# Performance work log

Hardware: AMD Instinct MI355X
Metric: run time of the kernel (lower is better)

Reference implementation:

```python
import jax, jax.numpy as jnp
import numpy as np

D = 1024      # d_model
E = 8         # num_experts
K = 2         # top_k
H = 4096      # expert_dim (bottleneck)
P = 256       # proj_dim
BATCH, SEQ = 2, 2048
CLAMP_MAX = float(np.log(1.0 / 0.01))
INIT_T = 0.5


def setup_inputs() -> dict:
    key = jax.random.key(0)
    ks = jax.random.split(key, 6)
    x = jax.random.normal(ks[0], (BATCH, SEQ, D), jnp.float32)
    # cosine projector (nn.Linear default init ~ U(-1/sqrt(D), 1/sqrt(D)))
    lim = 1.0 / np.sqrt(D)
    Wp = jax.random.uniform(ks[1], (P, D), jnp.float32, -lim, lim)
    bp = jnp.zeros((P,), jnp.float32)
    sim = 0.01 * jax.random.normal(ks[2], (P, E), jnp.float32)
    temp = jnp.full((1,), np.log(1.0 / INIT_T), jnp.float32)
    # RepAdapter 1x1 convs == linear layers; xavier_uniform, zero bias
    bA = float(np.sqrt(6.0 / (D + H)))
    A = jax.random.uniform(ks[3], (E, H, D), jnp.float32, -bA, bA)
    a_bias = jnp.zeros((E, H), jnp.float32)
    Bw = jax.random.uniform(ks[4], (E, D, H), jnp.float32, -bA, bA)
    b_bias = jnp.zeros((E, D), jnp.float32)
    return dict(x=x, Wp=Wp, bp=bp, sim=sim, temp=temp, A=A, a_bias=a_bias, Bw=Bw, b_bias=b_bias)


def reference(x, Wp, bp, sim, temp, A, a_bias, Bw, b_bias):
    B, S, d = x.shape
    e = sim.shape[1]
    xf = x.reshape(-1, d)                                  # [T, D]
    # cosine gate
    proj = xf @ Wp.T + bp                                  # [T, P]
    projn = proj / jnp.maximum(jnp.linalg.norm(proj, axis=1, keepdims=True), 1e-12)
    simn = sim / jnp.maximum(jnp.linalg.norm(sim, axis=0, keepdims=True), 1e-12)
    scale = jnp.exp(jnp.minimum(temp, CLAMP_MAX))          # [1]
    gate_probs = jax.nn.softmax((projn @ simn) * scale, axis=-1)   # [T, E]
    topv, topi = jax.lax.top_k(gate_probs, K)              # [T, K]
    topv = topv / (topv.sum(axis=-1, keepdims=True) + 1e-8)
    # per-token per-expert combine weight
    w = jnp.sum(topv[:, :, None] * jax.nn.one_hot(topi, e, dtype=x.dtype), axis=1)  # [T, E]

    # experts: y_e(x) = x + B_e(A_e x + a_e) + b_e (no nonlinearity); combine weighted
    def body(acc, params):
        Ae, ab, Be, bb, we = params
        h = xf @ Ae.T + ab                                 # [T, H]
        f = h @ Be.T + bb                                  # [T, D]
        return acc + we[:, None] * (xf + f), None

    out, _ = jax.lax.scan(body, jnp.zeros_like(xf), (A, a_bias, Bw, b_bias, w.T))
    out = out.reshape(B, S, d)

    frac = gate_probs.mean(axis=0)                         # expert_fractions
    aux_loss = jnp.sum((frac - 1.0 / e) ** 2)
    usage = jnp.bincount(topi.reshape(-1), length=e).astype(jnp.float32)
    return out, aux_loss, frac, usage
```

## Files before the change

### kernel.cpp

```cpp
#include <hip/hip_runtime.h>
#include <stdint.h>


typedef __attribute__((ext_vector_type(4))) float floatx4;
typedef __attribute__((ext_vector_type(8))) short shortx8;
typedef unsigned short ushort_t;

#define T_TOKENS 4096
#define D_DIM    1024
#define E_EXP    8
#define H_DIM    4096
#define P_DIM    256
#define ROWS_PAD 10240
#define MBLK     40
#define MBLK1    80

__device__ __forceinline__ ushort_t f2bf(float f) {
  union { float f; unsigned int u; } c; c.f = f;
  unsigned int u = c.u;
  unsigned int r = u + 0x7FFFu + ((u >> 16) & 1u);
  return (ushort_t)(r >> 16);
}

__device__ __forceinline__ void stage16(const ushort_t* g, ushort_t* l) {
  __builtin_amdgcn_global_load_lds((const __attribute__((address_space(1))) void*)g,
                                   (__attribute__((address_space(3))) void*)l, 16, 0, 0);
}

__global__ __launch_bounds__(256) void k_cvt(const float* __restrict__ src,
                                             ushort_t* __restrict__ dst, int n4) {
  int g = blockIdx.x * 256 + threadIdx.x;
  if (g >= n4) return;
  floatx4 v = ((const floatx4*)src)[g];
  ushort4 o; o.x = f2bf(v.x); o.y = f2bf(v.y); o.z = f2bf(v.z); o.w = f2bf(v.w);
  ((ushort4*)dst)[g] = o;
}

__global__ __launch_bounds__(256) void k_small_init(int* counts, int* cursor,
                                                    float* frac_sum, int* row2tok) {
  int g = blockIdx.x * 256 + threadIdx.x;
  if (g < 8) { counts[g] = 0; cursor[g] = 0; frac_sum[g] = 0.f; }
  if (g < ROWS_PAD) row2tok[g] = -1;
}

__global__ __launch_bounds__(256) void k_proj(const float* __restrict__ x,
                                              const float* __restrict__ Wp,
                                              const float* __restrict__ bp,
                                              float* __restrict__ proj) {
  __shared__ float Wc[256 * 36];
  __shared__ float Xc[16 * 36];
  int tid = threadIdx.x;
  int t0 = blockIdx.x * 16;
  int cg = tid & 31, tg = tid >> 5;
  floatx4 acc[2][8];
#pragma unroll
  for (int a = 0; a < 2; a++)
#pragma unroll
    for (int b = 0; b < 8; b++) acc[a][b] = (floatx4){0.f, 0.f, 0.f, 0.f};
  for (int kc = 0; kc < 32; ++kc) {
    int k0 = kc * 32;
    __syncthreads();
#pragma unroll
    for (int it = 0; it < 8; ++it) {
      int f = it * 256 + tid;
      int j = f >> 3, kk = (f & 7) << 2;
      floatx4 v = *(const floatx4*)(Wp + j * 1024 + k0 + kk);
      *(floatx4*)(Wc + j * 36 + kk) = v;
    }
    if (tid < 128) {
      int t = tid >> 3, kk = (tid & 7) << 2;
      floatx4 v = *(const floatx4*)(x + (size_t)(t0 + t) * 1024 + k0 + kk);
      *(floatx4*)(Xc + t * 36 + kk) = v;
    }
    __syncthreads();
#pragma unroll
    for (int k4 = 0; k4 < 8; ++k4) {
      floatx4 xv[2], wv[8];
#pragma unroll
      for (int tt = 0; tt < 2; tt++) xv[tt] = *(floatx4*)(Xc + (tg * 2 + tt) * 36 + k4 * 4);
#pragma unroll
      for (int jj = 0; jj < 8; jj++) wv[jj] = *(floatx4*)(Wc + (cg + jj * 32) * 36 + k4 * 4);
#pragma unroll
      for (int tt = 0; tt < 2; tt++)
#pragma unroll
        for (int jj = 0; jj < 8; jj++) acc[tt][jj] += xv[tt] * wv[jj];
    }
  }
#pragma unroll
  for (int tt = 0; tt < 2; tt++)
#pragma unroll
    for (int jj = 0; jj < 8; jj++) {
      floatx4 a = acc[tt][jj];
      float s = (a.x + a.y) + (a.z + a.w);
      int t = t0 + tg * 2 + tt, j = cg + jj * 32;
      proj[t * 256 + j] = s + bp[j];
    }
}

__global__ __launch_bounds__(128) void k_gate(const float* __restrict__ proj,
                                              const float* __restrict__ sim,
                                              const float* __restrict__ temp,
                                              int* __restrict__ topi, float* __restrict__ wslot,
                                              float* __restrict__ swsum,
                                              float* __restrict__ frac_sum, int* __restrict__ counts) {
  __shared__ float simT[8][256];
  __shared__ float snorm[8];
  __shared__ float fracs[8];
  __shared__ int cnts[8];
  int tid = threadIdx.x;
  for (int i = tid; i < 2048; i += 128) { int p = i >> 3, e = i & 7; simT[e][p] = sim[i]; }
  if (tid < 8) { fracs[tid] = 0.f; cnts[tid] = 0; }
  __syncthreads();
  if (tid < 8) {
    float s = 0.f;
    for (int p = 0; p < 256; p++) { float v = simT[tid][p]; s += v * v; }
    snorm[tid] = fmaxf(sqrtf(s), 1e-12f);
  }
  __syncthreads();
  int t = blockIdx.x * 128 + tid;
  floatx4 n4 = (floatx4){0.f, 0.f, 0.f, 0.f};
  floatx4 d4[8];
#pragma unroll
  for (int e = 0; e < 8; e++) d4[e] = (floatx4){0.f, 0.f, 0.f, 0.f};
  const floatx4* pr = (const floatx4*)(proj + t * 256);
  for (int k4 = 0; k4 < 64; ++k4) {
    floatx4 p = pr[k4];
    n4 += p * p;
#pragma unroll
    for (int e = 0; e < 8; e++) d4[e] += p * *(const floatx4*)(&simT[e][k4 * 4]);
  }
  float nrm = fmaxf(sqrtf((n4.x + n4.y) + (n4.z + n4.w)), 1e-12f);
  float scale = expf(fminf(temp[0], 4.6051701859880914f));
  float pe[8];
  float mx = -1e30f;
#pragma unroll
  for (int e = 0; e < 8; e++) {
    float d = (d4[e].x + d4[e].y) + (d4[e].z + d4[e].w);
    pe[e] = d / (nrm * snorm[e]) * scale;
    mx = fmaxf(mx, pe[e]);
  }
  float sum = 0.f;
#pragma unroll
  for (int e = 0; e < 8; e++) { pe[e] = expf(pe[e] - mx); sum += pe[e]; }
#pragma unroll
  for (int e = 0; e < 8; e++) pe[e] /= sum;
  int i0 = 0;
#pragma unroll
  for (int e = 1; e < 8; e++) if (pe[e] > pe[i0]) i0 = e;
  int i1 = (i0 == 0) ? 1 : 0;
#pragma unroll
  for (int e = 0; e < 8; e++) if (e != i1 && e != i0 && pe[e] > pe[i1]) i1 = e;
  float v0 = pe[i0], v1 = pe[i1];
  float s2 = v0 + v1 + 1e-8f;
  float w0 = v0 / s2, w1 = v1 / s2;
  topi[t * 2] = i0; topi[t * 2 + 1] = i1;
  wslot[t * 2] = w0; wslot[t * 2 + 1] = w1;
  swsum[t] = w0 + w1;
#pragma unroll
  for (int e = 0; e < 8; e++) atomicAdd(&fracs[e], pe[e]);
  atomicAdd(&cnts[i0], 1); atomicAdd(&cnts[i1], 1);
  __syncthreads();
  if (tid < 8) { atomicAdd(&frac_sum[tid], fracs[tid]); atomicAdd(&counts[tid], cnts[tid]); }
}

__global__ void k_scan(const int* __restrict__ counts, const float* __restrict__ frac_sum,
                       int* __restrict__ offsets, int* __restrict__ blk2e,
                       float* __restrict__ out_tail) {
  __shared__ int offs[9];
  if (threadIdx.x == 0) {
    int off = 0;
    for (int e = 0; e < 8; e++) { offs[e] = off; off += ((counts[e] + 255) >> 8) << 8; }
    offs[8] = off;
    for (int e = 0; e < 9; e++) offsets[e] = offs[e];
    float aux = 0.f;
    for (int e = 0; e < 8; e++) { float fr = frac_sum[e] / 4096.f; aux += (fr - 0.125f) * (fr - 0.125f); }
    out_tail[0] = aux;
  }
  __syncthreads();
  int tid = threadIdx.x;
  if (tid < MBLK) {
    int r = tid * 256, e = -1;
    for (int q = 0; q < 8; q++) if (r >= offs[q] && r < offs[q + 1]) e = q;
    blk2e[tid] = e;
  }
  if (tid < 8) {
    out_tail[1 + tid] = frac_sum[tid] / 4096.f;
    out_tail[9 + tid] = (float)counts[tid];
  }
}

__global__ __launch_bounds__(256) void k_assign(const int* __restrict__ topi,
                                                const float* __restrict__ wslot,
                                                const int* __restrict__ offsets,
                                                int* __restrict__ cursor,
                                                int* __restrict__ row2tok, float* __restrict__ roww) {
  int g = blockIdx.x * 256 + threadIdx.x;
  if (g >= 8192) return;
  int t = g >> 1;
  int e = topi[g];
  int pos = atomicAdd(&cursor[e], 1);
  int r = offsets[e] + pos;
  row2tok[r] = t;
  roww[r] = wslot[g];
}

__global__ __launch_bounds__(64) void k_gather(const float* __restrict__ x,
                                               const int* __restrict__ row2tok,
                                               ushort_t* __restrict__ xg) {
  int r = blockIdx.x;
  int t = row2tok[r];
  ushort4* dst = (ushort4*)(xg + (size_t)r * 1024);
  if (t < 0) {
    ushort4 z; z.x = z.y = z.z = z.w = 0;
    for (int i = threadIdx.x; i < 256; i += 64) dst[i] = z;
  } else {
    const floatx4* src = (const floatx4*)(x + (size_t)t * 1024);
    for (int i = threadIdx.x; i < 256; i += 64) {
      floatx4 v = src[i];
      ushort4 o; o.x = f2bf(v.x); o.y = f2bf(v.y); o.z = f2bf(v.z); o.w = f2bf(v.w);
      dst[i] = o;
    }
  }
}

__global__ __launch_bounds__(256) void k_init_out(const float* __restrict__ x,
                                                  const float* __restrict__ swsum,
                                                  float* __restrict__ out) {
  int g = blockIdx.x * 256 + threadIdx.x;
  float s = swsum[g >> 8];
  floatx4 v = ((const floatx4*)x)[g];
  ((floatx4*)out)[g] = v * s;
}

__global__ __launch_bounds__(256, 2) void k_gemm1(const ushort_t* __restrict__ Aop0,
                                                  const ushort_t* __restrict__ Wall,
                                                  const float* __restrict__ bias,
                                                  const int* __restrict__ blk2e,
                                                  ushort_t* __restrict__ hout) {
  const int K = 1024, N = 4096;
  int gx = gridDim.x;
  int nwg = gx * gridDim.y;
  int flat = blockIdx.y * gx + blockIdx.x;
  int qq = nwg >> 3, rr = nwg & 7;
  int xcd = flat & 7, idx = flat >> 3;
  int swz = (xcd < rr ? xcd * (qq + 1) : rr * (qq + 1) + (xcd - rr) * qq) + idx;
  int rb = swz / gx, nb = swz - rb * gx;
  int e = blk2e[rb >> 1];
  if (e < 0) return;
  const ushort_t* Aop = Aop0 + (size_t)rb * 128 * K;
  const ushort_t* Bop = Wall + (size_t)e * N * K + (size_t)nb * 128 * K;

  __shared__ ushort_t As[2][8192], Bs[2][8192];

  int tid = threadIdx.x, lane = tid & 63, wv = tid >> 6;
  int l15 = lane & 15, q = lane >> 4;
  int wm = (wv & 1) << 6, wn = (wv >> 1) << 6;
  floatx4 acc[4][4];
#pragma unroll
  for (int i = 0; i < 4; i++)
#pragma unroll
    for (int j = 0; j < 4; j++) acc[i][j] = (floatx4){0.f, 0.f, 0.f, 0.f};

  int srow = tid >> 3, schunk = tid & 7;

  auto stage = [&](int kt, int buf) {
#pragma unroll
    for (int r = 0; r < 4; ++r) {
      int row = (r << 5) + srow;
      size_t goff = (size_t)row * K + (size_t)(kt << 6) + (size_t)((schunk ^ (row & 7)) << 3);
      int loff = ((r << 8) + (wv << 6)) << 3;
      stage16(Aop + goff, &As[buf][loff]);
      stage16(Bop + goff, &Bs[buf][loff]);
    }
  };

  stage(0, 0);
  __syncthreads();
  int cur = 0;
  for (int kt = 0; kt < 16; ++kt) {
    if (kt + 1 < 16) stage(kt + 1, cur ^ 1);
    const ushort_t* Ab = As[cur];
    const ushort_t* Bb = Bs[cur];
#pragma unroll
    for (int kc = 0; kc < 2; ++kc) {
      int cw = (kc << 2) + q;
      shortx8 af[4], bfv[4];
#pragma unroll
      for (int i = 0; i < 4; ++i) {
        int row = wm + i * 16 + l15;
        af[i] = *(const shortx8*)(Ab + (row << 6) + ((cw ^ (row & 7)) << 3));
      }
#pragma unroll
      for (int j = 0; j < 4; ++j) {
        int row = wn + j * 16 + l15;
        bfv[j] = *(const shortx8*)(Bb + (row << 6) + ((cw ^ (row & 7)) << 3));
      }
#pragma unroll
      for (int i = 0; i < 4; ++i)
#pragma unroll
        for (int j = 0; j < 4; ++j)
          acc[i][j] = __builtin_amdgcn_mfma_f32_16x16x32_bf16(af[i], bfv[j], acc[i][j], 0, 0, 0);
    }
    __syncthreads();
    cur ^= 1;
  }

  const float* be = bias + (size_t)e * N + (size_t)nb * 128;
  ushort_t* hp = hout + (size_t)(rb * 128) * N + (size_t)nb * 128;
#pragma unroll
  for (int j = 0; j < 4; ++j) {
    int n = wn + j * 16 + l15;
    float bv = be[n];
#pragma unroll
    for (int i = 0; i < 4; ++i)
#pragma unroll
      for (int r = 0; r < 4; ++r) {
        int m = wm + i * 16 + (q << 2) + r;
        hp[(size_t)m * N + n] = f2bf(acc[i][j][r] + bv);
      }
  }
}

__global__ __launch_bounds__(512, 2) void k_gemm2(const ushort_t* __restrict__ Aop0,
                                                  const ushort_t* __restrict__ Wall,
                                                  const float* __restrict__ bias,
                                                  const int* __restrict__ blk2e,
                                                  int K, int N,
                                                  float* __restrict__ outp,
                                                  const int* __restrict__ row2tok,
                                                  const float* __restrict__ roww) {
  int gx = gridDim.x;
  int nwg = gx * gridDim.y;
  int flat = blockIdx.y * gx + blockIdx.x;
  int qq = nwg >> 3, rr = nwg & 7;
  int xcd = flat & 7, idx = flat >> 3;
  int swz = (xcd < rr ? xcd * (qq + 1) : rr * (qq + 1) + (xcd - rr) * qq) + idx;
  int rb = swz / gx, nb = swz - rb * gx;

  int e = blk2e[rb];
  if (e < 0) return;
  int Kslice = K / gridDim.z;
  int kbase = blockIdx.z * Kslice;
  const ushort_t* Aop = Aop0 + (size_t)rb * 256 * K + kbase;
  const ushort_t* Bop = Wall + (size_t)e * N * K + (size_t)nb * 256 * K + kbase;

  __shared__ ushort_t As[2][16384], Bs[2][16384];

  int tid = threadIdx.x, lane = tid & 63, wv = tid >> 6;
  int l15 = lane & 15, q = lane >> 4;
  int wm = (wv >> 2) << 7;
  int wn = (wv & 3) << 6;

  floatx4 acc[8][4];
#pragma unroll
  for (int i = 0; i < 8; i++)
#pragma unroll
    for (int j = 0; j < 4; j++) acc[i][j] = (floatx4){0.f, 0.f, 0.f, 0.f};

  int srow = tid >> 3;
  int schunk = tid & 7;
  int ksteps = Kslice >> 6;
  int cur = 0;

  auto stage = [&](int kt, int buf) {
#pragma unroll
    for (int r = 0; r < 4; ++r) {
      int row = (r << 6) + srow;
      size_t goff = (size_t)row * K + (size_t)(kt << 6) + (size_t)((schunk ^ (row & 7)) << 3);
      int loff = ((r << 9) + (wv << 6)) << 3;
      stage16(Aop + goff, &As[buf][loff]);
      stage16(Bop + goff, &Bs[buf][loff]);
    }
  };

  stage(0, 0);
  __syncthreads();
  for (int ks = 0; ks < ksteps; ++ks) {
    if (ks + 1 < ksteps) stage(ks + 1, cur ^ 1);
    const ushort_t* Ab = As[cur];
    const ushort_t* Bb = Bs[cur];
#pragma unroll
    for (int kc = 0; kc < 2; ++kc) {
      int cw = (kc << 2) + q;
      shortx8 af[8], bfv[4];
#pragma unroll
      for (int i = 0; i < 8; ++i) {
        int row = wm + i * 16 + l15;
        af[i] = *(const shortx8*)(Ab + (row << 6) + ((cw ^ (row & 7)) << 3));
      }
#pragma unroll
      for (int j = 0; j < 4; ++j) {
        int row = wn + j * 16 + l15;
        bfv[j] = *(const shortx8*)(Bb + (row << 6) + ((cw ^ (row & 7)) << 3));
      }
#pragma unroll
      for (int i = 0; i < 8; ++i)
#pragma unroll
        for (int j = 0; j < 4; ++j)
          acc[i][j] = __builtin_amdgcn_mfma_f32_16x16x32_bf16(af[i], bfv[j], acc[i][j], 0, 0, 0);
    }
    __syncthreads();
    cur ^= 1;
  }

  const float* be = bias + (size_t)e * N + (size_t)nb * 256;
  bool addb = (blockIdx.z == 0);
  float bvv[4];
#pragma unroll
  for (int j = 0; j < 4; ++j) bvv[j] = addb ? be[wn + j * 16 + l15] : 0.f;
#pragma unroll
  for (int i = 0; i < 8; ++i)
#pragma unroll
    for (int r = 0; r < 4; ++r) {
      int m = wm + i * 16 + (q << 2) + r;
      int grow = rb * 256 + m;
      int tok = row2tok[grow];
      if (tok < 0) continue;
      float w = roww[grow];
      float* op = outp + (size_t)tok * 1024 + nb * 256;
#pragma unroll
      for (int j = 0; j < 4; ++j) {
        int n = wn + j * 16 + l15;
        atomicAdd(op + n, (acc[i][j][r] + bvv[j]) * w);
      }
    }
}

extern "C" void kernel_launch(void* const* d_in, const int* in_sizes, int n_in,
                              void* d_out, int out_size, void* d_ws, size_t ws_size,
                              hipStream_t stream) {
  (void)in_sizes; (void)n_in; (void)out_size; (void)ws_size;
  const float* x      = (const float*)d_in[0];
  const float* Wp     = (const float*)d_in[1];
  const float* bp     = (const float*)d_in[2];
  const float* sim    = (const float*)d_in[3];
  const float* temp   = (const float*)d_in[4];
  const float* A      = (const float*)d_in[5];
  const float* a_bias = (const float*)d_in[6];
  const float* Bw     = (const float*)d_in[7];
  const float* b_bias = (const float*)d_in[8];
  float* out = (float*)d_out;

  char* ws = (char*)d_ws;
  ushort_t* Abf    = (ushort_t*)(ws);
  ushort_t* Bbf    = (ushort_t*)(ws + 67108864);
  ushort_t* xg     = (ushort_t*)(ws + 134217728);
  ushort_t* h      = (ushort_t*)(ws + 155189248);
  float*    proj   = (float*)   (ws + 239075328);
  int*      topi   = (int*)     (ws + 243269632);
  float*    wslot  = (float*)   (ws + 243302400);
  float*    swsum  = (float*)   (ws + 243335168);
  int*      row2tok= (int*)     (ws + 243351552);
  float*    roww   = (float*)   (ws + 243392512);
  int*      counts = (int*)     (ws + 243433472);
  int*      cursor = (int*)     (ws + 243433504);
  int*      offsets= (int*)     (ws + 243433536);
  int*      blk2e  = (int*)     (ws + 243433600);
  float*    fracs  = (float*)   (ws + 243433760);

  k_cvt<<<32768, 256, 0, stream>>>(A,  Abf, 8388608);
  k_cvt<<<32768, 256, 0, stream>>>(Bw, Bbf, 8388608);
  k_small_init<<<40, 256, 0, stream>>>(counts, cursor, fracs, row2tok);
  k_proj<<<256, 256, 0, stream>>>(x, Wp, bp, proj);
  k_gate<<<32, 128, 0, stream>>>(proj, sim, temp, topi, wslot, swsum, fracs, counts);
  k_scan<<<1, 128, 0, stream>>>(counts, fracs, offsets, blk2e, out + 4194304);
  k_assign<<<32, 256, 0, stream>>>(topi, wslot, offsets, cursor, row2tok, roww);
  k_gather<<<ROWS_PAD, 64, 0, stream>>>(x, row2tok, xg);
  k_init_out<<<4096, 256, 0, stream>>>(x, swsum, out);
  k_gemm1<<<dim3(32, MBLK1, 1), 256, 0, stream>>>(xg, Abf, a_bias, blk2e, h);
  k_gemm2<<<dim3(4, MBLK, 2), 512, 0, stream>>>(h, Bbf, b_bias, blk2e, 4096, 1024,
                                                out, row2tok, roww);
}
```

Measured before the change: 773.9 us.

## Shrink gemm2 tiles to 128x128 single-buffered, merge cvt launches, widen gather blocks

The second expert GEMM moves from 256x256 tiles with 512 threads and double-buffered LDS to 128x128 tiles with 256 threads, a single LDS buffer and more resident blocks per CU. The aim is more blocks and better occupancy to hide latency, but it gives up both the copy/compute overlap and the reuse per loaded tile. The two weight conversion kernels become one launch. The gather kernel now handles four rows per 256-thread block.

Result: faster. 736.5 us (-4.8%).

```diff
diff --git a/kernel.cpp b/kernel.cpp
--- a/kernel.cpp
+++ b/kernel.cpp
@@ -27,13 +27,17 @@
                                    (__attribute__((address_space(3))) void*)l, 16, 0, 0);
 }
 
-__global__ __launch_bounds__(256) void k_cvt(const float* __restrict__ src,
-                                             ushort_t* __restrict__ dst, int n4) {
+__global__ __launch_bounds__(256) void k_cvt2(const float* __restrict__ srcA,
+                                              const float* __restrict__ srcB,
+                                              ushort_t* __restrict__ dstA,
+                                              ushort_t* __restrict__ dstB) {
   int g = blockIdx.x * 256 + threadIdx.x;
-  if (g >= n4) return;
-  floatx4 v = ((const floatx4*)src)[g];
+  const float* s; ushort_t* d; int i;
+  if (g < 8388608) { s = srcA; d = dstA; i = g; }
+  else             { s = srcB; d = dstB; i = g - 8388608; }
+  floatx4 v = ((const floatx4*)s)[i];
   ushort4 o; o.x = f2bf(v.x); o.y = f2bf(v.y); o.z = f2bf(v.z); o.w = f2bf(v.w);
-  ((ushort4*)dst)[g] = o;
+  ((ushort4*)d)[i] = o;
 }
 
 __global__ __launch_bounds__(256) void k_small_init(int* counts, int* cursor,
@@ -204,18 +208,19 @@
   roww[r] = wslot[g];
 }
 
-__global__ __launch_bounds__(64) void k_gather(const float* __restrict__ x,
-                                               const int* __restrict__ row2tok,
-                                               ushort_t* __restrict__ xg) {
-  int r = blockIdx.x;
+__global__ __launch_bounds__(256) void k_gather(const float* __restrict__ x,
+                                                const int* __restrict__ row2tok,
+                                                ushort_t* __restrict__ xg) {
+  int r = blockIdx.x * 4 + (threadIdx.x >> 6);
+  int l = threadIdx.x & 63;
   int t = row2tok[r];
   ushort4* dst = (ushort4*)(xg + (size_t)r * 1024);
   if (t < 0) {
     ushort4 z; z.x = z.y = z.z = z.w = 0;
-    for (int i = threadIdx.x; i < 256; i += 64) dst[i] = z;
+    for (int i = l; i < 256; i += 64) dst[i] = z;
   } else {
     const floatx4* src = (const floatx4*)(x + (size_t)t * 1024);
-    for (int i = threadIdx.x; i < 256; i += 64) {
+    for (int i = l; i < 256; i += 64) {
       floatx4 v = src[i];
       ushort4 o; o.x = f2bf(v.x); o.y = f2bf(v.y); o.z = f2bf(v.z); o.w = f2bf(v.w);
       dst[i] = o;
@@ -321,7 +326,7 @@
   }
 }
 
-__global__ __launch_bounds__(512, 2) void k_gemm2(const ushort_t* __restrict__ Aop0,
+__global__ __launch_bounds__(256, 4) void k_gemm2(const ushort_t* __restrict__ Aop0,
                                                   const ushort_t* __restrict__ Wall,
                                                   const float* __restrict__ bias,
                                                   const int* __restrict__ blk2e,
@@ -337,93 +342,78 @@
   int swz = (xcd < rr ? xcd * (qq + 1) : rr * (qq + 1) + (xcd - rr) * qq) + idx;
   int rb = swz / gx, nb = swz - rb * gx;
 
-  int e = blk2e[rb];
+  int e = blk2e[rb >> 1];
   if (e < 0) return;
   int Kslice = K / gridDim.z;
   int kbase = blockIdx.z * Kslice;
-  const ushort_t* Aop = Aop0 + (size_t)rb * 256 * K + kbase;
-  const ushort_t* Bop = Wall + (size_t)e * N * K + (size_t)nb * 256 * K + kbase;
-
-  __shared__ ushort_t As[2][16384], Bs[2][16384];
+  const ushort_t* Aop = Aop0 + (size_t)rb * 128 * K + kbase;
+  const ushort_t* Bop = Wall + (size_t)e * N * K + (size_t)nb * 128 * K + kbase;
+
+  __shared__ ushort_t As[8192], Bs[8192];
 
   int tid = threadIdx.x, lane = tid & 63, wv = tid >> 6;
   int l15 = lane & 15, q = lane >> 4;
-  int wm = (wv >> 2) << 7;
-  int wn = (wv & 3) << 6;
-
-  floatx4 acc[8][4];
-#pragma unroll
-  for (int i = 0; i < 8; i++)
+  int wm = (wv & 1) << 6, wn = (wv >> 1) << 6;
+  floatx4 acc[4][4];
+#pragma unroll
+  for (int i = 0; i < 4; i++)
 #pragma unroll
     for (int j = 0; j < 4; j++) acc[i][j] = (floatx4){0.f, 0.f, 0.f, 0.f};
 
-  int srow = tid >> 3;
-  int schunk = tid & 7;
+  int srow = tid >> 3, schunk = tid & 7;
   int ksteps = Kslice >> 6;
-  int cur = 0;
-
-  auto stage = [&](int kt, int buf) {
+
+  for (int kt = 0; kt < ksteps; ++kt) {
 #pragma unroll
     for (int r = 0; r < 4; ++r) {
-      int row = (r << 6) + srow;
+      int row = (r << 5) + srow;
       size_t goff = (size_t)row * K + (size_t)(kt << 6) + (size_t)((schunk ^ (row & 7)) << 3);
-      int loff = ((r << 9) + (wv << 6)) << 3;
-      stage16(Aop + goff, &As[buf][loff]);
-      stage16(Bop + goff, &Bs[buf][loff]);
-    }
-  };
-
-  stage(0, 0);
-  __syncthreads();
-  for (int ks = 0; ks < ksteps; ++ks) {
-    if (ks + 1 < ksteps) stage(ks + 1, cur ^ 1);
-    const ushort_t* Ab = As[cur];
-    const ushort_t* Bb = Bs[cur];
+      int loff = ((r << 8) + (wv << 6)) << 3;
+      stage16(Aop + goff, &As[loff]);
+      stage16(Bop + goff, &Bs[loff]);
+    }
+    __syncthreads();
 #pragma unroll
     for (int kc = 0; kc < 2; ++kc) {
       int cw = (kc << 2) + q;
-      shortx8 af[8], bfv[4];
-#pragma unroll
-      for (int i = 0; i < 8; ++i) {
+      shortx8 af[4], bfv[4];
+#pragma unroll
+      for (int i = 0; i < 4; ++i) {
         int row = wm + i * 16 + l15;
-        af[i] = *(const shortx8*)(Ab + (row << 6) + ((cw ^ (row & 7)) << 3));
+        af[i] = *(const shortx8*)(As + (row << 6) + ((cw ^ (row & 7)) << 3));
       }
 #pragma unroll
       for (int j = 0; j < 4; ++j) {
         int row = wn + j * 16 + l15;
-        bfv[j] = *(const shortx8*)(Bb + (row << 6) + ((cw ^ (row & 7)) << 3));
-      }
-#pragma unroll
-      for (int i = 0; i < 8; ++i)
+        bfv[j] = *(const shortx8*)(Bs + (row << 6) + ((cw ^ (row & 7)) << 3));
+      }
+#pragma unroll
+      for (int i = 0; i < 4; ++i)
 #pragma unroll
         for (int j = 0; j < 4; ++j)
           acc[i][j] = __builtin_amdgcn_mfma_f32_16x16x32_bf16(af[i], bfv[j], acc[i][j], 0, 0, 0);
     }
     __syncthreads();
-    cur ^= 1;
-  }
-
-  const float* be = bias + (size_t)e * N + (size_t)nb * 256;
+  }
+
+  const float* be = bias + (size_t)e * N + (size_t)nb * 128;
   bool addb = (blockIdx.z == 0);
-  float bvv[4];
-#pragma unroll
-  for (int j = 0; j < 4; ++j) bvv[j] = addb ? be[wn + j * 16 + l15] : 0.f;
-#pragma unroll
-  for (int i = 0; i < 8; ++i)
-#pragma unroll
-    for (int r = 0; r < 4; ++r) {
-      int m = wm + i * 16 + (q << 2) + r;
-      int grow = rb * 256 + m;
-      int tok = row2tok[grow];
-      if (tok < 0) continue;
-      float w = roww[grow];
-      float* op = outp + (size_t)tok * 1024 + nb * 256;
-#pragma unroll
-      for (int j = 0; j < 4; ++j) {
-        int n = wn + j * 16 + l15;
-        atomicAdd(op + n, (acc[i][j][r] + bvv[j]) * w);
-      }
-    }
+#pragma unroll
+  for (int j = 0; j < 4; ++j) {
+    int n = wn + j * 16 + l15;
+    float bv = addb ? be[n] : 0.f;
+#pragma unroll
+    for (int i = 0; i < 4; ++i)
+#pragma unroll
+      for (int r = 0; r < 4; ++r) {
+        int m = wm + i * 16 + (q << 2) + r;
+        int grow = rb * 128 + m;
+        int tok = row2tok[grow];
+        if (tok < 0) continue;
+        float w = roww[grow];
+        atomicAdd(outp + (size_t)tok * 1024 + (size_t)nb * 128 + n, (acc[i][j][r] + bv) * w);
+      }
+  }
 }
 
 extern "C" void kernel_launch(void* const* d_in, const int* in_sizes, int n_in,
@@ -458,16 +448,15 @@
   int*      blk2e  = (int*)     (ws + 243433600);
   float*    fracs  = (float*)   (ws + 243433760);
 
-  k_cvt<<<32768, 256, 0, stream>>>(A,  Abf, 8388608);
-  k_cvt<<<32768, 256, 0, stream>>>(Bw, Bbf, 8388608);
+  k_cvt2<<<65536, 256, 0, stream>>>(A, Bw, Abf, Bbf);
   k_small_init<<<40, 256, 0, stream>>>(counts, cursor, fracs, row2tok);
   k_proj<<<256, 256, 0, stream>>>(x, Wp, bp, proj);
   k_gate<<<32, 128, 0, stream>>>(proj, sim, temp, topi, wslot, swsum, fracs, counts);
   k_scan<<<1, 128, 0, stream>>>(counts, fracs, offsets, blk2e, out + 4194304);
   k_assign<<<32, 256, 0, stream>>>(topi, wslot, offsets, cursor, row2tok, roww);
-  k_gather<<<ROWS_PAD, 64, 0, stream>>>(x, row2tok, xg);
+  k_gather<<<ROWS_PAD / 4, 256, 0, stream>>>(x, row2tok, xg);
   k_init_out<<<4096, 256, 0, stream>>>(x, swsum, out);
   k_gemm1<<<dim3(32, MBLK1, 1), 256, 0, stream>>>(xg, Abf, a_bias, blk2e, h);
-  k_gemm2<<<dim3(4, MBLK, 2), 512, 0, stream>>>(h, Bbf, b_bias, blk2e, 4096, 1024,
-                                                out, row2tok, roww);
-}
+  k_gemm2<<<dim3(8, MBLK1, 2), 256, 0, stream>>>(h, Bbf, b_bias, blk2e, 4096, 1024,
+                                                 out, row2tok, roww);
+}
```
